# Performance work log

Measured on AMD Instinct MI355X. Metric: run time of the kernel, lower is better.

The kernel has to match this reference:

```python
import jax, jax.numpy as jnp
import numpy as np

B, L, D, H = 8, 2048, 1024, 1024
BASE_LR, BASE_WD = 0.01, 0.9


def setup_inputs() -> dict:
    key = jax.random.key(0)
    ks = jax.random.split(key, 8)
    s = 1.0 / np.sqrt(D)
    return {
        "x": jax.random.normal(ks[0], (B, L, D), jnp.float32),
        "hidden": jax.random.normal(ks[1], (B, D, H), jnp.float32),
        "log_base_lr": jnp.array([np.log(BASE_LR)], jnp.float32),
        "w_lr": jax.random.normal(ks[2], (D, 1), jnp.float32) * s,
        "b_lr": jnp.zeros((1,), jnp.float32),
        "log_base_wd": jnp.array([np.log(BASE_WD)], jnp.float32),
        "w_wd": jax.random.normal(ks[3], (D, 1), jnp.float32) * s,
        "b_wd": jnp.zeros((1,), jnp.float32),
        "w_q": jax.random.normal(ks[4], (D, H), jnp.float32) * s,
        "b_q": jnp.zeros((H,), jnp.float32),
        "w_k": jax.random.normal(ks[5], (D, H), jnp.float32) * s,
        "b_k": jnp.zeros((H,), jnp.float32),
        "w_v": jax.random.normal(ks[6], (D, D), jnp.float32) * s,
        "b_v": jnp.zeros((D,), jnp.float32),
    }


def reference(x, hidden, log_base_lr, w_lr, b_lr, log_base_wd, w_wd, b_wd,
              w_q, b_q, w_k, b_k, w_v, b_v):
    batch, length, dim = x.shape
    W_prev = hidden  # [b, d, h]
    query = x @ w_q + b_q                     # [b, l, h]
    key = x @ w_k + b_k                       # [b, l, h]
    value = x @ w_v + b_v                     # [b, l, d]
    lr = jnp.exp(log_base_lr) * jax.nn.sigmoid((x @ w_lr + b_lr)[..., 0])  # [b, l]
    # log(1 - base_wd * sigmoid(.)) via log1p for stability; same math.
    log_wd = jnp.log1p(-jnp.exp(log_base_wd) * jax.nn.sigmoid((x @ w_wd + b_wd)[..., 0]))  # [b, l]
    wd_cross = jnp.exp(jnp.cumsum(log_wd, axis=1))  # [b, l]
    # inner-chunk decay: entry [b, m, l] = exp(sum_{j=m+1..l} log_wd[b, j]) for l >= m
    tri = jnp.triu(jnp.broadcast_to(log_wd[:, None, :], (batch, length, length)), k=1)
    wd_inner = jnp.triu(jnp.exp(jnp.cumsum(tri, axis=2)))  # [b, l, l]
    kq = jnp.einsum('bld,bmd->blm', key, query)            # [b, l, m]
    mask_kq = kq * wd_inner
    WpK_V = jnp.einsum('bdh,blh->bld', W_prev, key) - value  # [b, l, d]
    y_inner = -jnp.einsum('bld,bl,blm->bmd', WpK_V, lr, mask_kq)
    y_cross = jnp.einsum('bdh,blh,bl->bld', W_prev, query, wd_cross)
    y = y_inner + y_cross
    W_next_inner = -jnp.einsum('bld,bl,blh->bdh', WpK_V, lr * wd_inner[:, :, -1], key)
    W_next_cross = W_prev * wd_cross[:, -1][:, None, None]
    W_next = W_next_inner + W_next_cross
    return y, W_next
```

## Files before the change

kernel.cpp:

```cpp
#include <hip/hip_runtime.h>
#include <stdint.h>

#define BB 8
#define LL 2048
#define DD 1024
#define HH 1024
#define BL (BB*LL)

typedef __attribute__((ext_vector_type(8))) short short8;
typedef __attribute__((ext_vector_type(4))) float f32x4;

__device__ __forceinline__ unsigned short f2bf(float f) {
  unsigned int x = __float_as_uint(f);
  unsigned int r = (x + 0x7fffu + ((x >> 16) & 1u)) >> 16;
  return (unsigned short)r;
}
__device__ __forceinline__ float bf2f(unsigned short u) {
  return __uint_as_float(((unsigned int)u) << 16);
}

__device__ __forceinline__ void stage16(const unsigned short* g, unsigned short* l) {
  __builtin_amdgcn_global_load_lds((const __attribute__((address_space(1))) void*)g,
                                   (__attribute__((address_space(3))) void*)l,
                                   16, 0, 0);
}

template<int MI>
struct __align__(16) SmemT {
  unsigned short a[2][MI*2048];
  unsigned short b[2][16384];
};

template<int MI>
__device__ __forceinline__ void acc_initT(f32x4 (&acc)[MI][4]) {
#pragma unroll
  for (int i = 0; i < MI; ++i)
#pragma unroll
    for (int j = 0; j < 4; ++j)
      acc[i][j] = (f32x4){0.f, 0.f, 0.f, 0.f};
}

#define SCB __builtin_amdgcn_sched_barrier(0)

template<int MI, class FA, class FB>
__device__ __forceinline__ void gemm9_core(FA srcA, FB srcB, int NK,
                                           SmemT<MI>* sm, f32x4 (&acc)[MI][4]) {
  const int lane = threadIdx.x & 63;
  const int wave = threadIdx.x >> 6;
  const int srow = lane >> 3;
  const int scol = ((lane & 7) ^ srow) * 8;
  const int fk = (lane >> 4) * 8;
  const int fr = lane & 15;
  const int fx = fr & 7;
  const int mwr = (wave >> 2) * (MI * 16);
  const int nwr = (wave & 3) * 64;
  const int cA0 = (MI == 8) ? ((wave < 4) ? 2 * wave : 2 * wave + 8) : 2 * wave;
  const int cA1 = cA0 + 8;
  const int cB0 = (wave >> 1) * 8 + 2 * (wave & 1);
  const int cB1 = cB0 + 4;
  const int kc0 = (((fk >> 3) ^ fx) << 3);
  const int kc1 = ((((32 + fk) >> 3) ^ fx) << 3);

  auto SA2 = [&](int p, int kt, int c) {
    stage16(srcA(c * 8 + srow, kt) + scol, &sm->a[p][c * 512]);
    stage16(srcA(c * 8 + 8 + srow, kt) + scol, &sm->a[p][(c + 1) * 512]);
  };
  auto SB2 = [&](int p, int kt, int c) {
    stage16(srcB(c * 8 + srow, kt) + scol, &sm->b[p][c * 512]);
    stage16(srcB(c * 8 + 8 + srow, kt) + scol, &sm->b[p][(c + 1) * 512]);
  };

  short8 af0[4], af1[4], bfv[4][2];
  auto LDB4 = [&](int p, int kk, int kc) {
#pragma unroll
    for (int j = 0; j < 4; ++j)
      bfv[j][kk] = *(const short8*)&sm->b[p][(nwr + j * 16 + fr) * 64 + kc];
  };
  auto LDA4 = [&](short8 (&dst)[4], int p, int iho, int kc) {
#pragma unroll
    for (int i = 0; i < 4; ++i)
      dst[i] = *(const short8*)&sm->a[p][(mwr + iho + i * 16 + fr) * 64 + kc];
  };
  auto MM16 = [&](short8 (&a4)[4], int accb, int kk) {
#pragma unroll
    for (int i = 0; i < 4; ++i)
#pragma unroll
      for (int j = 0; j < 4; ++j)
        acc[accb + i][j] = __builtin_amdgcn_mfma_f32_16x16x32_bf16(
            a4[i], bfv[j][kk], acc[accb + i][j], 0, 0, 0);
  };

  SA2(0, 0, cA0);
  if (MI == 8) SA2(0, 0, cA1);
  SB2(0, 0, cB0); SB2(0, 0, cB1);
  if (NK > 1) {
    SB2(1, 1, cB0); SB2(1, 1, cB1);
    asm volatile("s_waitcnt vmcnt(4)" ::: "memory");
  } else {
    asm volatile("s_waitcnt vmcnt(0)" ::: "memory");
  }
  SCB; __builtin_amdgcn_s_barrier(); SCB;

  for (int t = 0; t < NK; ++t) {
    const int p = t & 1, po = p ^ 1;
    const bool s1 = (t + 1 < NK), s2 = (t + 2 < NK);
    if (s1) { SA2(po, t + 1, cA0); if (MI == 8) SA2(po, t + 1, cA1); }
    if constexpr (MI == 8) {
      LDB4(p, 0, kc0);
      LDA4(af0, p, 0, kc0);
      LDA4(af1, p, 64, kc0);
      asm volatile("s_waitcnt lgkmcnt(4)" ::: "memory"); SCB;
      __builtin_amdgcn_s_setprio(1); MM16(af0, 0, 0); __builtin_amdgcn_s_setprio(0);
      LDB4(p, 1, kc1);
      LDA4(af0, p, 0, kc1);
      asm volatile("s_waitcnt lgkmcnt(8)" ::: "memory"); SCB;
      __builtin_amdgcn_s_setprio(1); MM16(af1, 4, 0); __builtin_amdgcn_s_setprio(0);
      LDA4(af1, p, 64, kc1);
      asm volatile("s_waitcnt lgkmcnt(4)" ::: "memory"); SCB;
      __builtin_amdgcn_s_setprio(1); MM16(af0, 0, 1); __builtin_amdgcn_s_setprio(0);
      SCB; __builtin_amdgcn_s_barrier(); SCB;
      if (s2) { SB2(p, t + 2, cB0); SB2(p, t + 2, cB1); }
      asm volatile("s_waitcnt lgkmcnt(0)" ::: "memory"); SCB;
      __builtin_amdgcn_s_setprio(1); MM16(af1, 4, 1); __builtin_amdgcn_s_setprio(0);
      SCB;
    } else {
      LDB4(p, 0, kc0);
      LDA4(af0, p, 0, kc0);
      LDB4(p, 1, kc1);
      LDA4(af1, p, 0, kc1);
      asm volatile("s_waitcnt lgkmcnt(8)" ::: "memory"); SCB;
      __builtin_amdgcn_s_setprio(1); MM16(af0, 0, 0); __builtin_amdgcn_s_setprio(0);
      asm volatile("s_waitcnt lgkmcnt(0)" ::: "memory"); SCB;
      SCB; __builtin_amdgcn_s_barrier(); SCB;
      if (s2) { SB2(p, t + 2, cB0); SB2(p, t + 2, cB1); }
      __builtin_amdgcn_s_setprio(1); MM16(af1, 0, 1); __builtin_amdgcn_s_setprio(0);
      SCB;
    }
    if (s2)      { asm volatile("s_waitcnt vmcnt(4)" ::: "memory"); }
    else if (s1) { asm volatile("s_waitcnt vmcnt(0)" ::: "memory"); }
    SCB; __builtin_amdgcn_s_barrier(); SCB;
  }
}

template<int MI, typename F>
__device__ __forceinline__ void epiT(const f32x4 (&acc)[MI][4], F body) {
  const int lane = threadIdx.x & 63;
  const int wave = threadIdx.x >> 6;
  const int mwr = (wave >> 2) * (MI * 16), nwr = (wave & 3) * 64;
#pragma unroll
  for (int i = 0; i < MI; ++i)
#pragma unroll
    for (int j = 0; j < 4; ++j)
#pragma unroll
      for (int jj = 0; jj < 4; ++jj)
        body(mwr + i * 16 + ((lane >> 4) << 2) + jj,
             nwr + j * 16 + (lane & 15), acc[i][j][jj]);
}


__global__ void k_zero(float4* __restrict__ p) {
  p[(size_t)blockIdx.x * 256 + threadIdx.x] = make_float4(0.f, 0.f, 0.f, 0.f);
}

__global__ void k_prep_x(const float* __restrict__ x, const float* __restrict__ wlr,
                         const float* __restrict__ wwd, unsigned short* __restrict__ xb,
                         float* __restrict__ lrlog, float* __restrict__ wdlog) {
  const int wave = threadIdx.x >> 6, lane = threadIdx.x & 63;
  const int row = blockIdx.x * 4 + wave;
  const float* xr = x + (size_t)row * DD;
  float s1 = 0.f, s2 = 0.f;
#pragma unroll
  for (int ch = 0; ch < 4; ++ch) {
    const int col = ch * 256 + lane * 4;
    float4 v = *(const float4*)(xr + col);
    float4 a = *(const float4*)(wlr + col);
    float4 b = *(const float4*)(wwd + col);
    s1 += v.x*a.x + v.y*a.y + v.z*a.z + v.w*a.w;
    s2 += v.x*b.x + v.y*b.y + v.z*b.z + v.w*b.w;
    uint2 u;
    u.x = (unsigned)f2bf(v.x) | ((unsigned)f2bf(v.y) << 16);
    u.y = (unsigned)f2bf(v.z) | ((unsigned)f2bf(v.w) << 16);
    *(uint2*)(xb + (size_t)row * DD + col) = u;
  }
#pragma unroll
  for (int off = 32; off > 0; off >>= 1) {
    s1 += __shfl_down(s1, off);
    s2 += __shfl_down(s2, off);
  }
  if (lane == 0) { lrlog[row] = s1; wdlog[row] = s2; }
}

__global__ void k_prep_w(const float* __restrict__ wq, const float* __restrict__ wk,
                         const float* __restrict__ wv, unsigned short* __restrict__ wqt,
                         unsigned short* __restrict__ wkt, unsigned short* __restrict__ wvtn,
                         unsigned short* __restrict__ wkr) {
  const int idx = blockIdx.x * 256 + threadIdx.x;
  if (blockIdx.z == 3) { wkr[idx] = f2bf(wk[idx]); return; }
  const int k = idx >> 10, n = idx & 1023;
  const float* src = (blockIdx.z == 0) ? wq : (blockIdx.z == 1) ? wk : wv;
  unsigned short* dst = (blockIdx.z == 0) ? wqt : (blockIdx.z == 1) ? wkt : wvtn;
  float v = src[(size_t)k * 1024 + n];
  if (blockIdx.z == 2) v = -v;
  dst[(size_t)n * 1024 + k] = f2bf(v);
}

__global__ void k_prep_h(const float* __restrict__ hid, unsigned short* __restrict__ wpb) {
  const size_t i = ((size_t)blockIdx.x * 256 + threadIdx.x) * 4;
  float4 v = *(const float4*)(hid + i);
  uint2 u;
  u.x = (unsigned)f2bf(v.x) | ((unsigned)f2bf(v.y) << 16);
  u.y = (unsigned)f2bf(v.z) | ((unsigned)f2bf(v.w) << 16);
  *(uint2*)(wpb + i) = u;
}

__global__ void k_bias2(const unsigned short* __restrict__ wpb, const float* __restrict__ bk,
                        const float* __restrict__ bv, float* __restrict__ bias2) {
  const int wave = threadIdx.x >> 6, lane = threadIdx.x & 63;
  const int row = blockIdx.x * 4 + wave;
  const unsigned short* wr = wpb + (size_t)row * HH;
  float s = 0.f;
#pragma unroll
  for (int ch = 0; ch < 4; ++ch) {
    const int col = ch * 256 + lane * 4;
    float4 a = *(const float4*)(bk + col);
    ushort4 u = *(const ushort4*)(wr + col);
    s += a.x * bf2f(u.x) + a.y * bf2f(u.y) + a.z * bf2f(u.z) + a.w * bf2f(u.w);
  }
#pragma unroll
  for (int off = 32; off > 0; off >>= 1) s += __shfl_down(s, off);
  if (lane == 0) bias2[row] = s - bv[row & 1023];
}

__global__ void k_scan(const float* __restrict__ lrlog, const float* __restrict__ wdlog,
                       const float* __restrict__ lbl, const float* __restrict__ blr,
                       const float* __restrict__ lbw, const float* __restrict__ bwd,
                       float* __restrict__ lr, float* __restrict__ c,
                       float* __restrict__ s, float* __restrict__ ecl) {
  const int b = blockIdx.x, t = threadIdx.x;
  __shared__ float sums[256];
  const float elr = expf(lbl[0]);
  const float ewd = expf(lbw[0]);
  const float blr0 = blr[0], bwd0 = bwd[0];
  float lw[8];
  const float* wb = wdlog + (size_t)b * LL + t * 8;
  float tot = 0.f;
#pragma unroll
  for (int i = 0; i < 8; ++i) {
    float z = wb[i] + bwd0;
    float sig = 1.f / (1.f + expf(-z));
    tot += log1pf(-ewd * sig);
    lw[i] = tot;
  }
  sums[t] = tot;
  __syncthreads();
  for (int off = 1; off < 256; off <<= 1) {
    float v = (t >= off) ? sums[t - off] : 0.f;
    __syncthreads();
    sums[t] += v;
    __syncthreads();
  }
  const float prev = (t > 0) ? sums[t - 1] : 0.f;
  const float ctot = sums[255];
  const float* lb = lrlog + (size_t)b * LL + t * 8;
#pragma unroll
  for (int i = 0; i < 8; ++i) {
    const int idx = b * LL + t * 8 + i;
    const float ci = prev + lw[i];
    c[idx] = ci;
    float zl = lb[i] + blr0;
    float lri = elr / (1.f + expf(-zl));
    lr[idx] = lri;
    s[idx] = lri * expf(ctot - ci);
  }
  if (t == 0) ecl[b] = expf(ctot);
}


__global__ __launch_bounds__(512, 2) void k9_gemm_m2(const unsigned short* __restrict__ wpb,
    const unsigned short* __restrict__ wkr, const unsigned short* __restrict__ wvtn,
    unsigned short* __restrict__ w2t) {
  __shared__ SmemT<4> sm;
  const int b = blockIdx.x;
  const int mt = blockIdx.y & 7, nt = blockIdx.y >> 3;
  const int m0 = mt * 128, n0 = nt * 256;
  f32x4 acc[4][4]; acc_initT<4>(acc);
  gemm9_core<4>(
    [&](int r, int kt) { return wpb + (size_t)b * DD * HH + (size_t)(m0 + r) * HH + kt * 64; },
    [&](int r, int kt) { return wkr + (size_t)(n0 + r) * HH + kt * 64; },
    HH / 64, &sm, acc);
  epiT<4>(acc, [&](int rr, int cc, float av) {
    const size_t gi = (size_t)(m0 + rr) * DD + (n0 + cc);
    w2t[(size_t)b * DD * DD + gi] = f2bf(av + bf2f(wvtn[gi]));
  });
}

__global__ __launch_bounds__(512, 2) void k9_gemm_q(const unsigned short* __restrict__ xb,
    const unsigned short* __restrict__ wt, const float* __restrict__ bias,
    const float* __restrict__ c, unsigned short* __restrict__ outb,
    unsigned short* __restrict__ q2b) {
  __shared__ SmemT<8> sm;
  const int mt = blockIdx.x * 8 + (blockIdx.y & 7);
  const int nt = blockIdx.y >> 3;
  const int m0 = mt * 256, n0 = nt * 256;
  f32x4 acc[8][4]; acc_initT<8>(acc);
  gemm9_core<8>(
    [&](int r, int kt) { return xb + (size_t)(m0 + r) * DD + kt * 64; },
    [&](int r, int kt) { return wt + (size_t)(n0 + r) * DD + kt * 64; },
    DD / 64, &sm, acc);
  const int lane = threadIdx.x & 63, wave = threadIdx.x >> 6;
  const int mwr = (wave >> 2) * 128, nwr = (wave & 3) * 64;
  float er[8][4];
#pragma unroll
  for (int i = 0; i < 8; ++i)
#pragma unroll
    for (int jj = 0; jj < 4; ++jj)
      er[i][jj] = __expf(c[m0 + mwr + i * 16 + ((lane >> 4) << 2) + jj]);
#pragma unroll
  for (int i = 0; i < 8; ++i)
#pragma unroll
    for (int j = 0; j < 4; ++j)
#pragma unroll
      for (int jj = 0; jj < 4; ++jj) {
        const int row = m0 + mwr + i * 16 + ((lane >> 4) << 2) + jj;
        const int col = n0 + nwr + j * 16 + (lane & 15);
        const float v = acc[i][j][jj] + bias[col];
        outb[(size_t)row * HH + col] = f2bf(v);
        q2b[(size_t)row * HH + col] = f2bf(v * er[i][jj]);
      }
}

__global__ __launch_bounds__(512, 2) void k9_gemm_k(const unsigned short* __restrict__ xb,
    const unsigned short* __restrict__ wt, const float* __restrict__ bias,
    const float* __restrict__ s, unsigned short* __restrict__ kb,
    unsigned short* __restrict__ k2t) {
  __shared__ SmemT<8> sm;
  const int mt = blockIdx.x * 8 + (blockIdx.y & 7);
  const int nt = blockIdx.y >> 3;
  const int m0 = mt * 256, n0 = nt * 256;
  f32x4 acc[8][4]; acc_initT<8>(acc);
  gemm9_core<8>(
    [&](int r, int kt) { return xb + (size_t)(m0 + r) * DD + kt * 64; },
    [&](int r, int kt) { return wt + (size_t)(n0 + r) * DD + kt * 64; },
    DD / 64, &sm, acc);
  const int lane = threadIdx.x & 63, wave = threadIdx.x >> 6;
  const int mwr = (wave >> 2) * 128, nwr = (wave & 3) * 64;
#pragma unroll
  for (int i = 0; i < 8; ++i)
#pragma unroll
    for (int j = 0; j < 4; ++j) {
      const int col = n0 + nwr + j * 16 + (lane & 15);
      const float bias_c = bias[col];
      const int row0 = m0 + mwr + i * 16 + ((lane >> 4) << 2);
      const int b = row0 >> 11, ml0 = row0 & 2047;
      unsigned short tmp[4];
#pragma unroll
      for (int jj = 0; jj < 4; ++jj) {
        float v = acc[i][j][jj] + bias_c;
        kb[(size_t)(row0 + jj) * HH + col] = f2bf(v);
        tmp[jj] = f2bf(v * s[row0 + jj]);
      }
      uint2 u;
      u.x = (unsigned)tmp[0] | ((unsigned)tmp[1] << 16);
      u.y = (unsigned)tmp[2] | ((unsigned)tmp[3] << 16);
      *(uint2*)&k2t[((size_t)b * HH + col) * LL + ml0] = u;
    }
}

__global__ __launch_bounds__(512, 2) void k9_gemm_u(const unsigned short* __restrict__ xb,
    const unsigned short* __restrict__ w2t, const float* __restrict__ bias2,
    unsigned short* __restrict__ ut) {
  __shared__ SmemT<8> sm;
  const int b = blockIdx.x;
  const int mt = blockIdx.x * 8 + (blockIdx.y & 7);
  const int nt = blockIdx.y >> 3;
  const int m0 = mt * 256, n0 = nt * 256;
  f32x4 acc[8][4]; acc_initT<8>(acc);
  gemm9_core<8>(
    [&](int r, int kt) { return xb + (size_t)(m0 + r) * DD + kt * 64; },
    [&](int r, int kt) { return w2t + (size_t)b * DD * DD + (size_t)(n0 + r) * DD + kt * 64; },
    DD / 64, &sm, acc);
  const int lane = threadIdx.x & 63, wave = threadIdx.x >> 6;
  const int mwr = (wave >> 2) * 128, nwr = (wave & 3) * 64;
#pragma unroll
  for (int i = 0; i < 8; ++i)
#pragma unroll
    for (int j = 0; j < 4; ++j) {
      const int col = n0 + nwr + j * 16 + (lane & 15);
      const float b2c = bias2[b * DD + col];
      const int row0 = m0 + mwr + i * 16 + ((lane >> 4) << 2);
      const int ml0 = row0 & 2047;
      unsigned short tmp[4];
#pragma unroll
      for (int jj = 0; jj < 4; ++jj) tmp[jj] = f2bf(acc[i][j][jj] + b2c);
      uint2 u;
      u.x = (unsigned)tmp[0] | ((unsigned)tmp[1] << 16);
      u.y = (unsigned)tmp[2] | ((unsigned)tmp[3] << 16);
      *(uint2*)&ut[((size_t)b * DD + col) * LL + ml0] = u;
    }
}

__global__ __launch_bounds__(512, 2) void k9_gemm_p(const unsigned short* __restrict__ qb,
    const unsigned short* __restrict__ kb, const float* __restrict__ lr,
    const float* __restrict__ c, unsigned short* __restrict__ pb) {
  __shared__ SmemT<8> sm;
  const int b = blockIdx.x;
  const int t = blockIdx.y;
  int mt = (int)((sqrtf(8.f * (float)t + 1.f) - 1.f) * 0.5f);
  while ((mt + 1) * (mt + 2) / 2 <= t) ++mt;
  while (mt * (mt + 1) / 2 > t) --mt;
  const int nt = t - mt * (mt + 1) / 2;
  const int base = b * LL;
  const int m0 = mt * 256, n0 = nt * 256;
  f32x4 acc[8][4]; acc_initT<8>(acc);
  gemm9_core<8>(
    [&](int rr, int kt) { return qb + (size_t)(base + m0 + rr) * HH + kt * 64; },
    [&](int rr, int kt) { return kb + (size_t)(base + n0 + rr) * HH + kt * 64; },
    HH / 64, &sm, acc);
  const int lane = threadIdx.x & 63, wave = threadIdx.x >> 6;
  const int mwr = (wave >> 2) * 128, nwr = (wave & 3) * 64;
  if (nt != mt) {
    const float cref = c[base + m0];
    float er[8][4], fc[4];
#pragma unroll
    for (int i = 0; i < 8; ++i)
#pragma unroll
      for (int jj = 0; jj < 4; ++jj)
        er[i][jj] = __expf(c[base + m0 + mwr + i * 16 + ((lane >> 4) << 2) + jj] - cref);
#pragma unroll
    for (int j = 0; j < 4; ++j) {
      const int l = n0 + nwr + j * 16 + (lane & 15);
      fc[j] = lr[base + l] * __expf(cref - c[base + l]);
    }
#pragma unroll
    for (int i = 0; i < 8; ++i)
#pragma unroll
      for (int j = 0; j < 4; ++j) {
        const int l = n0 + nwr + j * 16 + (lane & 15);
        const int row0 = m0 + mwr + i * 16 + ((lane >> 4) << 2);
#pragma unroll
        for (int jj = 0; jj < 4; ++jj) {
          const float v = -acc[i][j][jj] * er[i][jj] * fc[j];
          pb[((size_t)base + row0 + jj) * LL + l] = f2bf(v);
        }
      }
  } else {
    epiT<8>(acc, [&](int rr, int cc, float av) {
      const int m = m0 + rr, l = n0 + cc;
      float v = 0.f;
      if (l <= m) v = -av * lr[base + l] * __expf(c[base + m] - c[base + l]);
      pb[((size_t)base + m) * LL + l] = f2bf(v);
    });
  }
}

__global__ __launch_bounds__(512, 2) void k9_gemm_y(const unsigned short* __restrict__ pb,
    const unsigned short* __restrict__ ut, const unsigned short* __restrict__ q2b,
    const unsigned short* __restrict__ wpb, float* __restrict__ out) {
  __shared__ SmemT<8> sm;
  const int b = blockIdx.x;
  const int sr = blockIdx.y & 7, nt = blockIdx.y >> 3;
  const int n0 = nt * 256;
  const unsigned short* pbB = pb + (size_t)b * LL * LL;
  const unsigned short* utB = ut + (size_t)b * DD * LL;
  const unsigned short* q2B = q2b + (size_t)b * LL * HH;
  const unsigned short* wpB = wpb + (size_t)b * DD * HH;
  f32x4 acc[8][4];
#pragma unroll
  for (int job = 0; job < 2; ++job) {
    const int mt = job ? (7 - sr) : sr;
    const int m0 = mt * 256;
    const int H = (mt + 1) * 2;
    const int pk0 = job ? H : 0;
    const int qk0 = job ? 8 : 0;
    acc_initT<8>(acc);
    gemm9_core<8>(
      [&](int r, int kt) { return pbB + (size_t)(m0 + r) * LL + (pk0 + kt) * 64; },
      [&](int r, int kt) { return utB + (size_t)(n0 + r) * LL + (pk0 + kt) * 64; },
      H, &sm, acc);
    gemm9_core<8>(
      [&](int r, int kt) { return q2B + (size_t)(m0 + r) * HH + (qk0 + kt) * 64; },
      [&](int r, int kt) { return wpB + (size_t)(n0 + r) * HH + (qk0 + kt) * 64; },
      8, &sm, acc);
    epiT<8>(acc, [&](int rr, int cc, float av) {
      unsafeAtomicAdd(&out[((size_t)b * LL + m0 + rr) * DD + (n0 + cc)], av);
    });
    asm volatile("s_waitcnt vmcnt(0)" ::: "memory");
    SCB;
  }
}

__global__ __launch_bounds__(512, 2) void k9_gemm_wn(const unsigned short* __restrict__ ut,
    const unsigned short* __restrict__ k2t, const float* __restrict__ hid,
    const float* __restrict__ ecl, float* __restrict__ out2) {
  __shared__ SmemT<4> sm;
  const int b = blockIdx.x;
  const int mt = blockIdx.y & 7, nt = blockIdx.y >> 3;
  const int m0 = mt * 128, n0 = nt * 256;
  f32x4 acc[4][4]; acc_initT<4>(acc);
  gemm9_core<4>(
    [&](int r, int kt) { return ut + (size_t)b * DD * LL + (size_t)(m0 + r) * LL + kt * 64; },
    [&](int r, int kt) { return k2t + (size_t)b * HH * LL + (size_t)(n0 + r) * LL + kt * 64; },
    LL / 64, &sm, acc);
  const float eclb = ecl[b];
  epiT<4>(acc, [&](int rr, int cc, float av) {
    const size_t gi = ((size_t)b * DD + (m0 + rr)) * HH + (n0 + cc);
    out2[gi] = -av + eclb * hid[gi];
  });
}


extern "C" void kernel_launch(void* const* d_in, const int* in_sizes, int n_in,
                              void* d_out, int out_size, void* d_ws, size_t ws_size,
                              hipStream_t stream) {
  (void)in_sizes; (void)n_in; (void)out_size; (void)ws_size;
  const float* x   = (const float*)d_in[0];
  const float* hid = (const float*)d_in[1];
  const float* lbl = (const float*)d_in[2];
  const float* wlr = (const float*)d_in[3];
  const float* blr = (const float*)d_in[4];
  const float* lbw = (const float*)d_in[5];
  const float* wwd = (const float*)d_in[6];
  const float* bwd = (const float*)d_in[7];
  const float* wq  = (const float*)d_in[8];
  const float* bq  = (const float*)d_in[9];
  const float* wk  = (const float*)d_in[10];
  const float* bk  = (const float*)d_in[11];
  const float* wv  = (const float*)d_in[12];
  const float* bv  = (const float*)d_in[13];
  float* out = (float*)d_out;

  char* w = (char*)d_ws;
  constexpr size_t SZ_XB  = (size_t)BL * DD * 2;
  constexpr size_t SZ_QB  = (size_t)BL * HH * 2;
  constexpr size_t SZ_KB  = (size_t)BL * HH * 2;
  constexpr size_t SZ_K2T = (size_t)BB * HH * LL * 2;
  constexpr size_t SZ_UT  = (size_t)BB * DD * LL * 2;
  constexpr size_t SZ_PB  = (size_t)BB * LL * LL * 2;
  constexpr size_t SZ_WT  = (size_t)DD * HH * 2;
  constexpr size_t SZ_WPB = (size_t)BB * DD * HH * 2;
  constexpr size_t SZ_V16 = (size_t)BL * 4;

  size_t off = 0;
  unsigned short* xb   = (unsigned short*)(w + off); off += SZ_XB;
  unsigned short* qb   = (unsigned short*)(w + off); off += SZ_QB;
  unsigned short* kb   = (unsigned short*)(w + off); off += SZ_KB;
  unsigned short* k2t  = (unsigned short*)(w + off); off += SZ_K2T;
  unsigned short* ut   = (unsigned short*)(w + off); off += SZ_UT;
  unsigned short* pb   = (unsigned short*)(w + off); off += SZ_PB;
  unsigned short* wqt  = (unsigned short*)(w + off); off += SZ_WT;
  unsigned short* wkt  = (unsigned short*)(w + off); off += SZ_WT;
  unsigned short* wvtn = (unsigned short*)(w + off); off += SZ_WT;
  unsigned short* wpb  = (unsigned short*)(w + off); off += SZ_WPB;
  float* lrlog = (float*)(w + off); off += SZ_V16;
  float* wdlog = (float*)(w + off); off += SZ_V16;
  float* lr    = (float*)(w + off); off += SZ_V16;
  float* c     = (float*)(w + off); off += SZ_V16;
  float* s     = (float*)(w + off); off += SZ_V16;
  float* ecl   = (float*)(w + off); off += 256;
  float* bias2 = (float*)(w + off); off += (size_t)BB * DD * 4;

  unsigned short* w2t = pb;
  unsigned short* wkr = pb + (size_t)BB * DD * DD;

  unsigned short* q2b = (unsigned short*)(out + (size_t)BL * DD);
  float* out2 = out + (size_t)BL * DD;

  k_zero<<<dim3(BL * DD / 4 / 256), 256, 0, stream>>>((float4*)out);
  k_prep_x<<<dim3(BL / 4), 256, 0, stream>>>(x, wlr, wwd, xb, lrlog, wdlog);
  k_prep_w<<<dim3(4096, 1, 4), 256, 0, stream>>>(wq, wk, wv, wqt, wkt, wvtn, wkr);
  k_prep_h<<<dim3((unsigned)((size_t)BB * DD * HH / 1024)), 256, 0, stream>>>(hid, wpb);
  k_scan<<<dim3(BB), 256, 0, stream>>>(lrlog, wdlog, lbl, blr, lbw, bwd, lr, c, s, ecl);
  k_bias2<<<dim3(BB * DD / 4), 256, 0, stream>>>(wpb, bk, bv, bias2);

  k9_gemm_m2<<<dim3(8, 32), 512, 0, stream>>>(wpb, wkr, wvtn, w2t);
  k9_gemm_q<<<dim3(8, 32), 512, 0, stream>>>(xb, wqt, bq, c, qb, q2b);
  k9_gemm_k<<<dim3(8, 32), 512, 0, stream>>>(xb, wkt, bk, s, kb, k2t);
  k9_gemm_u<<<dim3(8, 32), 512, 0, stream>>>(xb, w2t, bias2, ut);
  k9_gemm_p<<<dim3(8, 36), 512, 0, stream>>>(qb, kb, lr, c, pb);
  k9_gemm_y<<<dim3(8, 32), 512, 0, stream>>>(pb, ut, q2b, wpb, out);
  k9_gemm_wn<<<dim3(8, 32), 512, 0, stream>>>(ut, k2t, hid, ecl, out2);
}
```

Before: 675.1 us.

## Shrink attention GEMM tiles, fuse y K-loops, drop atomics and zero-fill

The causal P and Y GEMMs move from 256-row to 128-row tiles. Y now runs the P·U and Q2·Wp contractions as one concatenated K-loop and writes the output directly, so the separate zero-fill kernel and the atomic adds are gone. The core GEMM loop is simplified to load all of B up front and wait for lgkmcnt(0) before each MFMA group. The aim is better load balance across the triangular work and less memory traffic, at the cost of fewer overlapped LDS loads in the inner loop.

```diff
diff --git a/kernel.cpp b/kernel.cpp
--- a/kernel.cpp
+++ b/kernel.cpp
@@ -41,10 +41,11 @@
 }
 
 #define SCB __builtin_amdgcn_sched_barrier(0)
+#define LGKM0 do { asm volatile("s_waitcnt lgkmcnt(0)" ::: "memory"); SCB; } while (0)
 
 template<int MI, class FA, class FB>
-__device__ __forceinline__ void gemm9_core(FA srcA, FB srcB, int NK,
-                                           SmemT<MI>* sm, f32x4 (&acc)[MI][4]) {
+__device__ __forceinline__ void gemm10_core(FA srcA, FB srcB, int NK,
+                                            SmemT<MI>* sm, f32x4 (&acc)[MI][4]) {
   const int lane = threadIdx.x & 63;
   const int wave = threadIdx.x >> 6;
   const int srow = lane >> 3;
@@ -70,28 +71,30 @@
     stage16(srcB(c * 8 + 8 + srow, kt) + scol, &sm->b[p][(c + 1) * 512]);
   };
 
-  short8 af0[4], af1[4], bfv[4][2];
-  auto LDB4 = [&](int p, int kk, int kc) {
-#pragma unroll
-    for (int j = 0; j < 4; ++j)
-      bfv[j][kk] = *(const short8*)&sm->b[p][(nwr + j * 16 + fr) * 64 + kc];
+  short8 af[4], bfv[4][2];
+  auto LDB = [&](int p) {
+#pragma unroll
+    for (int j = 0; j < 4; ++j) {
+      bfv[j][0] = *(const short8*)&sm->b[p][(nwr + j * 16 + fr) * 64 + kc0];
+      bfv[j][1] = *(const short8*)&sm->b[p][(nwr + j * 16 + fr) * 64 + kc1];
+    }
   };
-  auto LDA4 = [&](short8 (&dst)[4], int p, int iho, int kc) {
+  auto LDA4 = [&](int p, int iho, int kc) {
 #pragma unroll
     for (int i = 0; i < 4; ++i)
-      dst[i] = *(const short8*)&sm->a[p][(mwr + iho + i * 16 + fr) * 64 + kc];
+      af[i] = *(const short8*)&sm->a[p][(mwr + iho + i * 16 + fr) * 64 + kc];
   };
-  auto MM16 = [&](short8 (&a4)[4], int accb, int kk) {
+  auto MMk = [&](int accb, int kk) {
 #pragma unroll
     for (int i = 0; i < 4; ++i)
 #pragma unroll
       for (int j = 0; j < 4; ++j)
         acc[accb + i][j] = __builtin_amdgcn_mfma_f32_16x16x32_bf16(
-            a4[i], bfv[j][kk], acc[accb + i][j], 0, 0, 0);
+            af[i], bfv[j][kk], acc[accb + i][j], 0, 0, 0);
   };
 
   SA2(0, 0, cA0);
-  if (MI == 8) SA2(0, 0, cA1);
+  if constexpr (MI == 8) SA2(0, 0, cA1);
   SB2(0, 0, cB0); SB2(0, 0, cB1);
   if (NK > 1) {
     SB2(1, 1, cB0); SB2(1, 1, cB1);
@@ -104,38 +107,31 @@
   for (int t = 0; t < NK; ++t) {
     const int p = t & 1, po = p ^ 1;
     const bool s1 = (t + 1 < NK), s2 = (t + 2 < NK);
-    if (s1) { SA2(po, t + 1, cA0); if (MI == 8) SA2(po, t + 1, cA1); }
+    if (s1) { SA2(po, t + 1, cA0); if constexpr (MI == 8) SA2(po, t + 1, cA1); }
+    LDB(p);
+    LDA4(p, 0, kc0);
+    LGKM0;
+    __builtin_amdgcn_s_setprio(1); MMk(0, 0); __builtin_amdgcn_s_setprio(0);
     if constexpr (MI == 8) {
-      LDB4(p, 0, kc0);
-      LDA4(af0, p, 0, kc0);
-      LDA4(af1, p, 64, kc0);
-      asm volatile("s_waitcnt lgkmcnt(4)" ::: "memory"); SCB;
-      __builtin_amdgcn_s_setprio(1); MM16(af0, 0, 0); __builtin_amdgcn_s_setprio(0);
-      LDB4(p, 1, kc1);
-      LDA4(af0, p, 0, kc1);
-      asm volatile("s_waitcnt lgkmcnt(8)" ::: "memory"); SCB;
-      __builtin_amdgcn_s_setprio(1); MM16(af1, 4, 0); __builtin_amdgcn_s_setprio(0);
-      LDA4(af1, p, 64, kc1);
-      asm volatile("s_waitcnt lgkmcnt(4)" ::: "memory"); SCB;
-      __builtin_amdgcn_s_setprio(1); MM16(af0, 0, 1); __builtin_amdgcn_s_setprio(0);
+      LDA4(p, 0, kc1);
+      LGKM0;
+      __builtin_amdgcn_s_setprio(1); MMk(0, 1); __builtin_amdgcn_s_setprio(0);
       SCB; __builtin_amdgcn_s_barrier(); SCB;
       if (s2) { SB2(p, t + 2, cB0); SB2(p, t + 2, cB1); }
-      asm volatile("s_waitcnt lgkmcnt(0)" ::: "memory"); SCB;
-      __builtin_amdgcn_s_setprio(1); MM16(af1, 4, 1); __builtin_amdgcn_s_setprio(0);
-      SCB;
+      LDA4(p, 64, kc0);
+      LGKM0;
+      __builtin_amdgcn_s_setprio(1); MMk(4, 0); __builtin_amdgcn_s_setprio(0);
+      LDA4(p, 64, kc1);
+      LGKM0;
+      __builtin_amdgcn_s_setprio(1); MMk(4, 1); __builtin_amdgcn_s_setprio(0);
     } else {
-      LDB4(p, 0, kc0);
-      LDA4(af0, p, 0, kc0);
-      LDB4(p, 1, kc1);
-      LDA4(af1, p, 0, kc1);
-      asm volatile("s_waitcnt lgkmcnt(8)" ::: "memory"); SCB;
-      __builtin_amdgcn_s_setprio(1); MM16(af0, 0, 0); __builtin_amdgcn_s_setprio(0);
-      asm volatile("s_waitcnt lgkmcnt(0)" ::: "memory"); SCB;
       SCB; __builtin_amdgcn_s_barrier(); SCB;
       if (s2) { SB2(p, t + 2, cB0); SB2(p, t + 2, cB1); }
-      __builtin_amdgcn_s_setprio(1); MM16(af1, 0, 1); __builtin_amdgcn_s_setprio(0);
-      SCB;
+      LDA4(p, 0, kc1);
+      LGKM0;
+      __builtin_amdgcn_s_setprio(1); MMk(0, 1); __builtin_amdgcn_s_setprio(0);
     }
+    SCB;
     if (s2)      { asm volatile("s_waitcnt vmcnt(4)" ::: "memory"); }
     else if (s1) { asm volatile("s_waitcnt vmcnt(0)" ::: "memory"); }
     SCB; __builtin_amdgcn_s_barrier(); SCB;
@@ -157,10 +153,6 @@
              nwr + j * 16 + (lane & 15), acc[i][j][jj]);
 }
 
-
-__global__ void k_zero(float4* __restrict__ p) {
-  p[(size_t)blockIdx.x * 256 + threadIdx.x] = make_float4(0.f, 0.f, 0.f, 0.f);
-}
 
 __global__ void k_prep_x(const float* __restrict__ x, const float* __restrict__ wlr,
                          const float* __restrict__ wwd, unsigned short* __restrict__ xb,
@@ -276,7 +268,7 @@
 }
 
 
-__global__ __launch_bounds__(512, 2) void k9_gemm_m2(const unsigned short* __restrict__ wpb,
+__global__ __launch_bounds__(512, 2) void k10_gemm_m2(const unsigned short* __restrict__ wpb,
     const unsigned short* __restrict__ wkr, const unsigned short* __restrict__ wvtn,
     unsigned short* __restrict__ w2t) {
   __shared__ SmemT<4> sm;
@@ -284,7 +276,7 @@
   const int mt = blockIdx.y & 7, nt = blockIdx.y >> 3;
   const int m0 = mt * 128, n0 = nt * 256;
   f32x4 acc[4][4]; acc_initT<4>(acc);
-  gemm9_core<4>(
+  gemm10_core<4>(
     [&](int r, int kt) { return wpb + (size_t)b * DD * HH + (size_t)(m0 + r) * HH + kt * 64; },
     [&](int r, int kt) { return wkr + (size_t)(n0 + r) * HH + kt * 64; },
     HH / 64, &sm, acc);
@@ -294,7 +286,7 @@
   });
 }
 
-__global__ __launch_bounds__(512, 2) void k9_gemm_q(const unsigned short* __restrict__ xb,
+__global__ __launch_bounds__(512, 2) void k10_gemm_q(const unsigned short* __restrict__ xb,
     const unsigned short* __restrict__ wt, const float* __restrict__ bias,
     const float* __restrict__ c, unsigned short* __restrict__ outb,
     unsigned short* __restrict__ q2b) {
@@ -303,7 +295,7 @@
   const int nt = blockIdx.y >> 3;
   const int m0 = mt * 256, n0 = nt * 256;
   f32x4 acc[8][4]; acc_initT<8>(acc);
-  gemm9_core<8>(
+  gemm10_core<8>(
     [&](int r, int kt) { return xb + (size_t)(m0 + r) * DD + kt * 64; },
     [&](int r, int kt) { return wt + (size_t)(n0 + r) * DD + kt * 64; },
     DD / 64, &sm, acc);
@@ -329,7 +321,7 @@
       }
 }
 
-__global__ __launch_bounds__(512, 2) void k9_gemm_k(const unsigned short* __restrict__ xb,
+__global__ __launch_bounds__(512, 2) void k10_gemm_k(const unsigned short* __restrict__ xb,
     const unsigned short* __restrict__ wt, const float* __restrict__ bias,
     const float* __restrict__ s, unsigned short* __restrict__ kb,
     unsigned short* __restrict__ k2t) {
@@ -338,7 +330,7 @@
   const int nt = blockIdx.y >> 3;
   const int m0 = mt * 256, n0 = nt * 256;
   f32x4 acc[8][4]; acc_initT<8>(acc);
-  gemm9_core<8>(
+  gemm10_core<8>(
     [&](int r, int kt) { return xb + (size_t)(m0 + r) * DD + kt * 64; },
     [&](int r, int kt) { return wt + (size_t)(n0 + r) * DD + kt * 64; },
     DD / 64, &sm, acc);
@@ -366,7 +358,7 @@
     }
 }
 
-__global__ __launch_bounds__(512, 2) void k9_gemm_u(const unsigned short* __restrict__ xb,
+__global__ __launch_bounds__(512, 2) void k10_gemm_u(const unsigned short* __restrict__ xb,
     const unsigned short* __restrict__ w2t, const float* __restrict__ bias2,
     unsigned short* __restrict__ ut) {
   __shared__ SmemT<8> sm;
@@ -375,7 +367,7 @@
   const int nt = blockIdx.y >> 3;
   const int m0 = mt * 256, n0 = nt * 256;
   f32x4 acc[8][4]; acc_initT<8>(acc);
-  gemm9_core<8>(
+  gemm10_core<8>(
     [&](int r, int kt) { return xb + (size_t)(m0 + r) * DD + kt * 64; },
     [&](int r, int kt) { return w2t + (size_t)b * DD * DD + (size_t)(n0 + r) * DD + kt * 64; },
     DD / 64, &sm, acc);
@@ -399,64 +391,37 @@
     }
 }
 
-__global__ __launch_bounds__(512, 2) void k9_gemm_p(const unsigned short* __restrict__ qb,
+__global__ __launch_bounds__(512, 2) void k10_gemm_p(const unsigned short* __restrict__ qb,
     const unsigned short* __restrict__ kb, const float* __restrict__ lr,
     const float* __restrict__ c, unsigned short* __restrict__ pb) {
-  __shared__ SmemT<8> sm;
+  __shared__ SmemT<4> sm;
   const int b = blockIdx.x;
   const int t = blockIdx.y;
-  int mt = (int)((sqrtf(8.f * (float)t + 1.f) - 1.f) * 0.5f);
-  while ((mt + 1) * (mt + 2) / 2 <= t) ++mt;
-  while (mt * (mt + 1) / 2 > t) --mt;
-  const int nt = t - mt * (mt + 1) / 2;
+  int r = (int)((sqrtf(4.f * (float)t + 1.f) - 1.f) * 0.5f);
+  while ((r + 1) * (r + 2) <= t) ++r;
+  while (r * (r + 1) > t) --r;
+  const int u = t - r * (r + 1);
+  const int mt = 2 * r + (u > r ? 1 : 0);
+  const int nt2 = (u > r) ? (u - r - 1) : u;
   const int base = b * LL;
-  const int m0 = mt * 256, n0 = nt * 256;
-  f32x4 acc[8][4]; acc_initT<8>(acc);
-  gemm9_core<8>(
+  const int m0 = mt * 128, n0 = nt2 * 256;
+  f32x4 acc[4][4]; acc_initT<4>(acc);
+  gemm10_core<4>(
     [&](int rr, int kt) { return qb + (size_t)(base + m0 + rr) * HH + kt * 64; },
     [&](int rr, int kt) { return kb + (size_t)(base + n0 + rr) * HH + kt * 64; },
     HH / 64, &sm, acc);
-  const int lane = threadIdx.x & 63, wave = threadIdx.x >> 6;
-  const int mwr = (wave >> 2) * 128, nwr = (wave & 3) * 64;
-  if (nt != mt) {
-    const float cref = c[base + m0];
-    float er[8][4], fc[4];
-#pragma unroll
-    for (int i = 0; i < 8; ++i)
-#pragma unroll
-      for (int jj = 0; jj < 4; ++jj)
-        er[i][jj] = __expf(c[base + m0 + mwr + i * 16 + ((lane >> 4) << 2) + jj] - cref);
-#pragma unroll
-    for (int j = 0; j < 4; ++j) {
-      const int l = n0 + nwr + j * 16 + (lane & 15);
-      fc[j] = lr[base + l] * __expf(cref - c[base + l]);
-    }
-#pragma unroll
-    for (int i = 0; i < 8; ++i)
-#pragma unroll
-      for (int j = 0; j < 4; ++j) {
-        const int l = n0 + nwr + j * 16 + (lane & 15);
-        const int row0 = m0 + mwr + i * 16 + ((lane >> 4) << 2);
-#pragma unroll
-        for (int jj = 0; jj < 4; ++jj) {
-          const float v = -acc[i][j][jj] * er[i][jj] * fc[j];
-          pb[((size_t)base + row0 + jj) * LL + l] = f2bf(v);
-        }
-      }
-  } else {
-    epiT<8>(acc, [&](int rr, int cc, float av) {
-      const int m = m0 + rr, l = n0 + cc;
-      float v = 0.f;
-      if (l <= m) v = -av * lr[base + l] * __expf(c[base + m] - c[base + l]);
-      pb[((size_t)base + m) * LL + l] = f2bf(v);
-    });
-  }
-}
-
-__global__ __launch_bounds__(512, 2) void k9_gemm_y(const unsigned short* __restrict__ pb,
+  epiT<4>(acc, [&](int rr, int cc, float av) {
+    const int m = m0 + rr, l = n0 + cc;
+    float v = 0.f;
+    if (l <= m) v = -av * lr[base + l] * __expf(c[base + m] - c[base + l]);
+    pb[((size_t)base + m) * LL + l] = f2bf(v);
+  });
+}
+
+__global__ __launch_bounds__(512, 2) void k10_gemm_y(const unsigned short* __restrict__ pb,
     const unsigned short* __restrict__ ut, const unsigned short* __restrict__ q2b,
     const unsigned short* __restrict__ wpb, float* __restrict__ out) {
-  __shared__ SmemT<8> sm;
+  __shared__ SmemT<4> sm;
   const int b = blockIdx.x;
   const int sr = blockIdx.y & 7, nt = blockIdx.y >> 3;
   const int n0 = nt * 256;
@@ -464,32 +429,30 @@
   const unsigned short* utB = ut + (size_t)b * DD * LL;
   const unsigned short* q2B = q2b + (size_t)b * LL * HH;
   const unsigned short* wpB = wpb + (size_t)b * DD * HH;
-  f32x4 acc[8][4];
+  f32x4 acc[4][4];
 #pragma unroll
   for (int job = 0; job < 2; ++job) {
-    const int mt = job ? (7 - sr) : sr;
-    const int m0 = mt * 256;
-    const int H = (mt + 1) * 2;
-    const int pk0 = job ? H : 0;
-    const int qk0 = job ? 8 : 0;
-    acc_initT<8>(acc);
-    gemm9_core<8>(
-      [&](int r, int kt) { return pbB + (size_t)(m0 + r) * LL + (pk0 + kt) * 64; },
-      [&](int r, int kt) { return utB + (size_t)(n0 + r) * LL + (pk0 + kt) * 64; },
-      H, &sm, acc);
-    gemm9_core<8>(
-      [&](int r, int kt) { return q2B + (size_t)(m0 + r) * HH + (qk0 + kt) * 64; },
-      [&](int r, int kt) { return wpB + (size_t)(n0 + r) * HH + (qk0 + kt) * 64; },
-      8, &sm, acc);
-    epiT<8>(acc, [&](int rr, int cc, float av) {
-      unsafeAtomicAdd(&out[((size_t)b * LL + m0 + rr) * DD + (n0 + cc)], av);
+    const int mt = job ? (15 - sr) : sr;
+    const int m0 = mt * 128;
+    const int NK1 = (mt + 1) * 2;
+    acc_initT<4>(acc);
+    gemm10_core<4>(
+      [&](int r, int kt) {
+        return (kt < NK1) ? pbB + (size_t)(m0 + r) * LL + kt * 64
+                          : q2B + (size_t)(m0 + r) * HH + (kt - NK1) * 64;
+      },
+      [&](int r, int kt) {
+        return (kt < NK1) ? utB + (size_t)(n0 + r) * LL + kt * 64
+                          : wpB + (size_t)(n0 + r) * HH + (kt - NK1) * 64;
+      },
+      NK1 + 16, &sm, acc);
+    epiT<4>(acc, [&](int rr, int cc, float av) {
+      out[((size_t)b * LL + m0 + rr) * DD + (n0 + cc)] = av;
     });
-    asm volatile("s_waitcnt vmcnt(0)" ::: "memory");
-    SCB;
-  }
-}
-
-__global__ __launch_bounds__(512, 2) void k9_gemm_wn(const unsigned short* __restrict__ ut,
+  }
+}
+
+__global__ __launch_bounds__(512, 2) void k10_gemm_wn(const unsigned short* __restrict__ ut,
     const unsigned short* __restrict__ k2t, const float* __restrict__ hid,
     const float* __restrict__ ecl, float* __restrict__ out2) {
   __shared__ SmemT<4> sm;
@@ -497,7 +460,7 @@
   const int mt = blockIdx.y & 7, nt = blockIdx.y >> 3;
   const int m0 = mt * 128, n0 = nt * 256;
   f32x4 acc[4][4]; acc_initT<4>(acc);
-  gemm9_core<4>(
+  gemm10_core<4>(
     [&](int r, int kt) { return ut + (size_t)b * DD * LL + (size_t)(m0 + r) * LL + kt * 64; },
     [&](int r, int kt) { return k2t + (size_t)b * HH * LL + (size_t)(n0 + r) * LL + kt * 64; },
     LL / 64, &sm, acc);
@@ -565,18 +528,17 @@
   unsigned short* q2b = (unsigned short*)(out + (size_t)BL * DD);
   float* out2 = out + (size_t)BL * DD;
 
-  k_zero<<<dim3(BL * DD / 4 / 256), 256, 0, stream>>>((float4*)out);
   k_prep_x<<<dim3(BL / 4), 256, 0, stream>>>(x, wlr, wwd, xb, lrlog, wdlog);
   k_prep_w<<<dim3(4096, 1, 4), 256, 0, stream>>>(wq, wk, wv, wqt, wkt, wvtn, wkr);
   k_prep_h<<<dim3((unsigned)((size_t)BB * DD * HH / 1024)), 256, 0, stream>>>(hid, wpb);
   k_scan<<<dim3(BB), 256, 0, stream>>>(lrlog, wdlog, lbl, blr, lbw, bwd, lr, c, s, ecl);
   k_bias2<<<dim3(BB * DD / 4), 256, 0, stream>>>(wpb, bk, bv, bias2);
 
-  k9_gemm_m2<<<dim3(8, 32), 512, 0, stream>>>(wpb, wkr, wvtn, w2t);
-  k9_gemm_q<<<dim3(8, 32), 512, 0, stream>>>(xb, wqt, bq, c, qb, q2b);
-  k9_gemm_k<<<dim3(8, 32), 512, 0, stream>>>(xb, wkt, bk, s, kb, k2t);
-  k9_gemm_u<<<dim3(8, 32), 512, 0, stream>>>(xb, w2t, bias2, ut);
-  k9_gemm_p<<<dim3(8, 36), 512, 0, stream>>>(qb, kb, lr, c, pb);
-  k9_gemm_y<<<dim3(8, 32), 512, 0, stream>>>(pb, ut, q2b, wpb, out);
-  k9_gemm_wn<<<dim3(8, 32), 512, 0, stream>>>(ut, k2t, hid, ecl, out2);
-}
+  k10_gemm_m2<<<dim3(8, 32), 512, 0, stream>>>(wpb, wkr, wvtn, w2t);
+  k10_gemm_q<<<dim3(8, 32), 512, 0, stream>>>(xb, wqt, bq, c, qb, q2b);
+  k10_gemm_k<<<dim3(8, 32), 512, 0, stream>>>(xb, wkt, bk, s, kb, k2t);
+  k10_gemm_u<<<dim3(8, 32), 512, 0, stream>>>(xb, w2t, bias2, ut);
+  k10_gemm_p<<<dim3(8, 72), 512, 0, stream>>>(qb, kb, lr, c, pb);
+  k10_gemm_y<<<dim3(8, 32), 512, 0, stream>>>(pb, ut, q2b, wpb, out);
+  k10_gemm_wn<<<dim3(8, 32), 512, 0, stream>>>(ut, k2t, hid, ecl, out2);
+}
```

Result: faster. 581.2 us (-13.9%).
